# Kernel optimization log

Hardware: AMD Instinct MI355X
Metric: run time of the kernel (lower is better)

## Reference

```python
import jax, jax.numpy as jnp
import numpy as np

W_VV = 0.5  # Eq. 5: mean of video-video and video-text similarity
W_VT = 0.5
MAX_K = 20
EPS = 1e-12  # matches torch.nn.functional.normalize default


def _l2norm(x):
    # normalize along last dim, clamping the norm like F.normalize
    n = jnp.linalg.norm(x, axis=-1, keepdims=True)
    return x / jnp.maximum(n, EPS)


def setup_inputs() -> dict:
    key = jax.random.key(0)
    k1, k2, k3 = jax.random.split(key, 3)
    B, N, D = 64, 100000, 1024
    z_ego = jax.random.normal(k1, (B, D), dtype=jnp.float32)
    exo_bank = jax.random.normal(k2, (N, D), dtype=jnp.float32)
    sim_vt = jax.random.uniform(k3, (N,), dtype=jnp.float32)
    return {"z_ego": z_ego, "exo_bank": exo_bank, "k": 20, "sim_vt": sim_vt}


def reference(z_ego, exo_bank, k, sim_vt):
    N = exo_bank.shape[0]
    k_eff = min(int(k), MAX_K, N)
    # pairwise cosine similarity: [B, N]
    sim_vv = _l2norm(z_ego) @ _l2norm(exo_bank).T
    # broadcast [N] video-text similarity to [B, N]
    sim_vt_b = jnp.broadcast_to(sim_vt[None, :], sim_vv.shape)
    score = W_VV * sim_vv + W_VT * sim_vt_b
    _, topk_idx = jax.lax.top_k(score, k_eff)  # [B, k_eff]
    z_exo = exo_bank[topk_idx]  # [B, k_eff, D]
    return z_exo, topk_idx
```

## Files before the change

kernel.cpp:

```cpp
#include <hip/hip_runtime.h>
#include <math.h>
#include <limits.h>

#define B 64
#define D 1024
#define MAXK 20
#define NSEG 8
#define NT 128
#define KC 64

#define IDX_SENT 0x7FFFFFFF
#define NEG_INF (-INFINITY)

__device__ __forceinline__ bool better(float av, int ai, float bv, int bi) {
    return (av > bv) || (av == bv && ai < bi);
}

__global__ __launch_bounds__(256) void k_norm_ego(const float* __restrict__ ego,
                                                  float* __restrict__ egoN) {
    const int b = blockIdx.x, t = threadIdx.x;
    float4 v = *(const float4*)(ego + (size_t)b * D + t * 4);
    float s = v.x * v.x + v.y * v.y + v.z * v.z + v.w * v.w;
#pragma unroll
    for (int m = 1; m < 64; m <<= 1) s += __shfl_xor(s, m);
    __shared__ float p[4];
    if ((t & 63) == 0) p[t >> 6] = s;
    __syncthreads();
    float tot = p[0] + p[1] + p[2] + p[3];
    float dnm = fmaxf(sqrtf(tot), 1e-12f);
    float4 o;
    o.x = v.x / dnm; o.y = v.y / dnm; o.z = v.z / dnm; o.w = v.w / dnm;
    *(float4*)(egoN + (size_t)b * D + t * 4) = o;
}

__global__ __launch_bounds__(256) void k_scores(const float* __restrict__ exo,
                                                const float* __restrict__ egoN,
                                                const float* __restrict__ svt,
                                                float* __restrict__ scores, int N) {
    __shared__ __align__(16) float eg[64 * 68];
    __shared__ __align__(16) float ex[128 * 64];
    __shared__ float nrm[128];

    const int t = threadIdx.x;
    const int jb = blockIdx.x * NT;
    const int tx = t & 15;
    const int ty = t >> 4;
    const int rr = t >> 4, cc = t & 15;

    float acc[4][8];
#pragma unroll
    for (int m = 0; m < 4; ++m)
#pragma unroll
        for (int i = 0; i < 8; ++i) acc[m][i] = 0.0f;
    float ssq[8] = {0, 0, 0, 0, 0, 0, 0, 0};

    for (int kc = 0; kc < D; kc += KC) {
        __syncthreads();
#pragma unroll
        for (int r = 0; r < 4; ++r) {
            int m = rr + 16 * r;
            float4 v = *(const float4*)(egoN + (size_t)m * D + kc + cc * 4);
            *(float4*)(eg + m * 68 + cc * 4) = v;
        }
#pragma unroll
        for (int r = 0; r < 8; ++r) {
            int j = rr + 16 * r;
            int jj = jb + j;
            float4 v = make_float4(0.f, 0.f, 0.f, 0.f);
            if (jj < N) v = *(const float4*)(exo + (size_t)jj * D + kc + cc * 4);
            ssq[r] += v.x * v.x + v.y * v.y + v.z * v.z + v.w * v.w;
            int cs = cc ^ ((j >> 3) & 7);
            *(float4*)(ex + (j << 6) + (cs << 2)) = v;
        }
        __syncthreads();

        const float* egp = eg + ty * 4 * 68;
#pragma unroll 4
        for (int k4 = 0; k4 < 16; ++k4) {
            float4 a0 = *(const float4*)(egp + 0 * 68 + k4 * 4);
            float4 a1 = *(const float4*)(egp + 1 * 68 + k4 * 4);
            float4 a2 = *(const float4*)(egp + 2 * 68 + k4 * 4);
            float4 a3 = *(const float4*)(egp + 3 * 68 + k4 * 4);
            int ko = (k4 ^ (tx & 7)) << 2;
#pragma unroll
            for (int i = 0; i < 8; ++i) {
                float4 e = *(const float4*)(ex + ((tx * 8 + i) << 6) + ko);
                acc[0][i] += a0.x * e.x; acc[0][i] += a0.y * e.y;
                acc[0][i] += a0.z * e.z; acc[0][i] += a0.w * e.w;
                acc[1][i] += a1.x * e.x; acc[1][i] += a1.y * e.y;
                acc[1][i] += a1.z * e.z; acc[1][i] += a1.w * e.w;
                acc[2][i] += a2.x * e.x; acc[2][i] += a2.y * e.y;
                acc[2][i] += a2.z * e.z; acc[2][i] += a2.w * e.w;
                acc[3][i] += a3.x * e.x; acc[3][i] += a3.y * e.y;
                acc[3][i] += a3.z * e.z; acc[3][i] += a3.w * e.w;
            }
        }
    }

#pragma unroll
    for (int r = 0; r < 8; ++r) {
        float s = ssq[r];
        s += __shfl_xor(s, 1); s += __shfl_xor(s, 2);
        s += __shfl_xor(s, 4); s += __shfl_xor(s, 8);
        if (cc == 0) nrm[rr + 16 * r] = s;
    }
    __syncthreads();

#pragma unroll
    for (int i = 0; i < 8; ++i) {
        int j = tx * 8 + i;
        int jj = jb + j;
        if (jj < N) {
            float dn = fmaxf(sqrtf(nrm[j]), 1e-12f);
            float sv = 0.5f * svt[jj];
#pragma unroll
            for (int m = 0; m < 4; ++m) {
                float sc = 0.5f * (acc[m][i] / dn) + sv;
                scores[(size_t)(ty * 4 + m) * N + jj] = sc;
            }
        }
    }
}

__global__ __launch_bounds__(256) void k_topk_scan(const float* __restrict__ scores,
                                                   float2* __restrict__ cand, int N) {
    const int row = blockIdx.x >> 3;
    const int seg = blockIdx.x & 7;
    const int t = threadIdx.x;
    const int seglen = (N + NSEG - 1) / NSEG;
    const int start = seg * seglen;
    const int end = (start + seglen < N) ? (start + seglen) : N;
    const float* rs = scores + (size_t)row * N;

    float lv[20]; int li[20];
#pragma unroll
    for (int p = 0; p < 20; ++p) { lv[p] = NEG_INF; li[p] = IDX_SENT; }

    for (int j = start + t; j < end; j += 256) {
        float s = rs[j];
        if (s > lv[19] || (s == lv[19] && j < li[19])) {
            float cv = s; int ci = j;
#pragma unroll
            for (int p = 0; p < 20; ++p) {
                bool bb = (cv > lv[p]) || (cv == lv[p] && ci < li[p]);
                float tv = lv[p]; int ti = li[p];
                lv[p] = bb ? cv : tv; li[p] = bb ? ci : ti;
                cv = bb ? tv : cv;   ci = bb ? ti : ci;
            }
        }
    }

    __shared__ float2 wc[4 * 20];
    const int lane = t & 63, w = t >> 6;
#pragma unroll 1
    for (int r = 0; r < 20; ++r) {
        float bv = lv[0]; int bi = li[0];
#pragma unroll
        for (int m = 1; m < 64; m <<= 1) {
            float ov = __shfl_xor(bv, m); int oi = __shfl_xor(bi, m);
            if (better(ov, oi, bv, bi)) { bv = ov; bi = oi; }
        }
        if (lv[0] == bv && li[0] == bi) {
#pragma unroll
            for (int p = 0; p < 19; ++p) { lv[p] = lv[p + 1]; li[p] = li[p + 1]; }
            lv[19] = NEG_INF; li[19] = IDX_SENT;
        }
        if (lane == 0) wc[w * 20 + r] = make_float2(bv, __int_as_float(bi));
    }
    __syncthreads();

    if (w == 0) {
        float mv[2]; int mi[2];
        float2 c0 = (lane < 80) ? wc[lane]
                                : make_float2(NEG_INF, __int_as_float(IDX_SENT));
        float2 c1 = (lane + 64 < 80) ? wc[lane + 64]
                                     : make_float2(NEG_INF, __int_as_float(IDX_SENT));
        mv[0] = c0.x; mi[0] = __float_as_int(c0.y);
        mv[1] = c1.x; mi[1] = __float_as_int(c1.y);
        if (better(mv[1], mi[1], mv[0], mi[0])) {
            float tv = mv[0]; int ti = mi[0];
            mv[0] = mv[1]; mi[0] = mi[1]; mv[1] = tv; mi[1] = ti;
        }
#pragma unroll 1
        for (int r = 0; r < 20; ++r) {
            float bv = mv[0]; int bi = mi[0];
#pragma unroll
            for (int m = 1; m < 64; m <<= 1) {
                float ov = __shfl_xor(bv, m); int oi = __shfl_xor(bi, m);
                if (better(ov, oi, bv, bi)) { bv = ov; bi = oi; }
            }
            if (mv[0] == bv && mi[0] == bi) {
                mv[0] = mv[1]; mi[0] = mi[1];
                mv[1] = NEG_INF; mi[1] = IDX_SENT;
            }
            if (lane == 0)
                cand[((size_t)row * NSEG + seg) * 20 + r] = make_float2(bv, __int_as_float(bi));
        }
    }
}

__global__ __launch_bounds__(64) void k_topk_final(const float2* __restrict__ cand,
                                                   int* __restrict__ idxi,
                                                   float* __restrict__ outIdx) {
    const int row = blockIdx.x;
    const int lane = threadIdx.x;
    const float2* c = cand + (size_t)row * NSEG * 20;

    float mv[3]; int mi[3];
#pragma unroll
    for (int s = 0; s < 3; ++s) { mv[s] = NEG_INF; mi[s] = IDX_SENT; }
#pragma unroll
    for (int s = 0; s < 3; ++s) {
        int ci = lane + 64 * s;
        if (ci < 160) { float2 cc = c[ci]; mv[s] = cc.x; mi[s] = __float_as_int(cc.y); }
    }
    {
        float tv; int ti;
        if (better(mv[1], mi[1], mv[0], mi[0])) { tv = mv[0]; ti = mi[0]; mv[0] = mv[1]; mi[0] = mi[1]; mv[1] = tv; mi[1] = ti; }
        if (better(mv[2], mi[2], mv[1], mi[1])) { tv = mv[1]; ti = mi[1]; mv[1] = mv[2]; mi[1] = mi[2]; mv[2] = tv; mi[2] = ti; }
        if (better(mv[1], mi[1], mv[0], mi[0])) { tv = mv[0]; ti = mi[0]; mv[0] = mv[1]; mi[0] = mi[1]; mv[1] = tv; mi[1] = ti; }
    }
#pragma unroll 1
    for (int r = 0; r < 20; ++r) {
        float bv = mv[0]; int bi = mi[0];
#pragma unroll
        for (int m = 1; m < 64; m <<= 1) {
            float ov = __shfl_xor(bv, m); int oi = __shfl_xor(bi, m);
            if (better(ov, oi, bv, bi)) { bv = ov; bi = oi; }
        }
        if (mv[0] == bv && mi[0] == bi) {
            mv[0] = mv[1]; mi[0] = mi[1];
            mv[1] = mv[2]; mi[1] = mi[2];
            mv[2] = NEG_INF; mi[2] = IDX_SENT;
        }
        if (lane == 0) {
            idxi[row * 20 + r] = bi;
            outIdx[row * 20 + r] = (float)bi;
        }
    }
}

__global__ __launch_bounds__(256) void k_gather(const float* __restrict__ exo,
                                                const int* __restrict__ idxi,
                                                float* __restrict__ out) {
    const int b = blockIdx.x / MAXK, s = blockIdx.x % MAXK;
    const int idx = idxi[b * MAXK + s];
    const float4* src = (const float4*)(exo + (size_t)idx * D);
    float4* dst = (float4*)(out + (size_t)(b * MAXK + s) * D);
    dst[threadIdx.x] = src[threadIdx.x];
}

extern "C" void kernel_launch(void* const* d_in, const int* in_sizes, int n_in,
                              void* d_out, int out_size, void* d_ws, size_t ws_size,
                              hipStream_t stream) {
    (void)n_in; (void)out_size; (void)ws_size;
    const float* ego = (const float*)d_in[0];
    const float* exo = (const float*)d_in[1];
    const float* svt = (const float*)d_in[3];
    const int N = in_sizes[1] / D;

    float* ws = (float*)d_ws;
    float* egoN = ws;
    float* scores = ws + (size_t)B * D;
    float2* cand = (float2*)(scores + (size_t)B * N);
    int* idxi = (int*)(cand + B * NSEG * 20);

    float* out = (float*)d_out;
    float* outIdx = out + (size_t)B * MAXK * D;

    k_norm_ego<<<B, 256, 0, stream>>>(ego, egoN);
    const int nblk = (N + NT - 1) / NT;
    k_scores<<<nblk, 256, 0, stream>>>(exo, egoN, svt, scores, N);
    k_topk_scan<<<B * NSEG, 256, 0, stream>>>(scores, cand, N);
    k_topk_final<<<B, 64, 0, stream>>>(cand, idxi, outIdx);
    k_gather<<<B * MAXK, 256, 0, stream>>>(exo, idxi, out);
}
```

Baseline: 860.6 us.

## Restructure score GEMM tiling with register prefetch and vectorize top-k scan

The score kernel now stages K-major transposed tiles of both operands in shared memory with KC=32. Each thread computes an 8x4 outer-product block from one float4 of exo and two float4s of ego, and the next chunk's global loads are prefetched into registers while the current chunk is computed. The epilogue writes scores as float4, and launch bounds request 4 blocks per CU. The top-k scan reads scores as float4 with 4-aligned segment boundaries, which cuts load instructions but gives each thread four consecutive elements instead of a strided one.

New measurement: 766.6 us. -10.9%, faster.

```diff
diff --git a/kernel.cpp b/kernel.cpp
--- a/kernel.cpp
+++ b/kernel.cpp
@@ -1,13 +1,14 @@
 #include <hip/hip_runtime.h>
 #include <math.h>
-#include <limits.h>
 
 #define B 64
 #define D 1024
 #define MAXK 20
 #define NSEG 8
 #define NT 128
-#define KC 64
+#define KC 32
+#define EXSTRIDE 132
+#define EGSTRIDE 68
 
 #define IDX_SENT 0x7FFFFFFF
 #define NEG_INF (-INFINITY)
@@ -33,91 +34,133 @@
     *(float4*)(egoN + (size_t)b * D + t * 4) = o;
 }
 
-__global__ __launch_bounds__(256) void k_scores(const float* __restrict__ exo,
-                                                const float* __restrict__ egoN,
-                                                const float* __restrict__ svt,
-                                                float* __restrict__ scores, int N) {
-    __shared__ __align__(16) float eg[64 * 68];
-    __shared__ __align__(16) float ex[128 * 64];
-    __shared__ float nrm[128];
+__global__ __launch_bounds__(256, 4) void k_scores(const float* __restrict__ exo,
+                                                   const float* __restrict__ egoN,
+                                                   const float* __restrict__ svt,
+                                                   float* __restrict__ scores, int N) {
+    __shared__ __align__(16) float ex[KC * EXSTRIDE];
+    __shared__ __align__(16) float eg[KC * EGSTRIDE];
+    __shared__ float nrm[NT];
 
     const int t = threadIdx.x;
     const int jb = blockIdx.x * NT;
-    const int tx = t & 15;
-    const int ty = t >> 4;
-    const int rr = t >> 4, cc = t & 15;
-
-    float acc[4][8];
-#pragma unroll
-    for (int m = 0; m < 4; ++m)
-#pragma unroll
-        for (int i = 0; i < 8; ++i) acc[m][i] = 0.0f;
-    float ssq[8] = {0, 0, 0, 0, 0, 0, 0, 0};
-
-    for (int kc = 0; kc < D; kc += KC) {
+    const int tx = t & 31;
+    const int ty = t >> 5;
+    const int jr = t >> 3;
+    const int kq = t & 7;
+
+    float4 acc[8];
+#pragma unroll
+    for (int m = 0; m < 8; ++m) acc[m] = make_float4(0.f, 0.f, 0.f, 0.f);
+    float ssq[4] = {0.f, 0.f, 0.f, 0.f};
+
+    float4 pe[4], pg[2];
+
+    const float4* ex4 = (const float4*)ex;
+    const float4* eg4 = (const float4*)eg;
+
+    {
+        const int kc = 0;
+#pragma unroll
+        for (int q = 0; q < 4; ++q) {
+            int j = jb + jr + 32 * q;
+            pe[q] = (j < N) ? *(const float4*)(exo + (size_t)j * D + kc + kq * 4)
+                            : make_float4(0.f, 0.f, 0.f, 0.f);
+        }
+#pragma unroll
+        for (int p2 = 0; p2 < 2; ++p2) {
+            int m = jr + 32 * p2;
+            pg[p2] = *(const float4*)(egoN + (size_t)m * D + kc + kq * 4);
+        }
+    }
+
+    for (int c = 0; c < D / KC; ++c) {
         __syncthreads();
 #pragma unroll
-        for (int r = 0; r < 4; ++r) {
-            int m = rr + 16 * r;
-            float4 v = *(const float4*)(egoN + (size_t)m * D + kc + cc * 4);
-            *(float4*)(eg + m * 68 + cc * 4) = v;
-        }
-#pragma unroll
-        for (int r = 0; r < 8; ++r) {
-            int j = rr + 16 * r;
-            int jj = jb + j;
-            float4 v = make_float4(0.f, 0.f, 0.f, 0.f);
-            if (jj < N) v = *(const float4*)(exo + (size_t)jj * D + kc + cc * 4);
-            ssq[r] += v.x * v.x + v.y * v.y + v.z * v.z + v.w * v.w;
-            int cs = cc ^ ((j >> 3) & 7);
-            *(float4*)(ex + (j << 6) + (cs << 2)) = v;
+        for (int q = 0; q < 4; ++q) {
+            ssq[q] += pe[q].x * pe[q].x + pe[q].y * pe[q].y +
+                      pe[q].z * pe[q].z + pe[q].w * pe[q].w;
+            int jl = jr + 32 * q;
+            ex[(kq * 4 + 0) * EXSTRIDE + jl] = pe[q].x;
+            ex[(kq * 4 + 1) * EXSTRIDE + jl] = pe[q].y;
+            ex[(kq * 4 + 2) * EXSTRIDE + jl] = pe[q].z;
+            ex[(kq * 4 + 3) * EXSTRIDE + jl] = pe[q].w;
+        }
+#pragma unroll
+        for (int p2 = 0; p2 < 2; ++p2) {
+            int ml = jr + 32 * p2;
+            eg[(kq * 4 + 0) * EGSTRIDE + ml] = pg[p2].x;
+            eg[(kq * 4 + 1) * EGSTRIDE + ml] = pg[p2].y;
+            eg[(kq * 4 + 2) * EGSTRIDE + ml] = pg[p2].z;
+            eg[(kq * 4 + 3) * EGSTRIDE + ml] = pg[p2].w;
         }
         __syncthreads();
-
-        const float* egp = eg + ty * 4 * 68;
-#pragma unroll 4
-        for (int k4 = 0; k4 < 16; ++k4) {
-            float4 a0 = *(const float4*)(egp + 0 * 68 + k4 * 4);
-            float4 a1 = *(const float4*)(egp + 1 * 68 + k4 * 4);
-            float4 a2 = *(const float4*)(egp + 2 * 68 + k4 * 4);
-            float4 a3 = *(const float4*)(egp + 3 * 68 + k4 * 4);
-            int ko = (k4 ^ (tx & 7)) << 2;
-#pragma unroll
-            for (int i = 0; i < 8; ++i) {
-                float4 e = *(const float4*)(ex + ((tx * 8 + i) << 6) + ko);
-                acc[0][i] += a0.x * e.x; acc[0][i] += a0.y * e.y;
-                acc[0][i] += a0.z * e.z; acc[0][i] += a0.w * e.w;
-                acc[1][i] += a1.x * e.x; acc[1][i] += a1.y * e.y;
-                acc[1][i] += a1.z * e.z; acc[1][i] += a1.w * e.w;
-                acc[2][i] += a2.x * e.x; acc[2][i] += a2.y * e.y;
-                acc[2][i] += a2.z * e.z; acc[2][i] += a2.w * e.w;
-                acc[3][i] += a3.x * e.x; acc[3][i] += a3.y * e.y;
-                acc[3][i] += a3.z * e.z; acc[3][i] += a3.w * e.w;
+        if (c + 1 < D / KC) {
+            const int kc = (c + 1) * KC;
+#pragma unroll
+            for (int q = 0; q < 4; ++q) {
+                int j = jb + jr + 32 * q;
+                pe[q] = (j < N) ? *(const float4*)(exo + (size_t)j * D + kc + kq * 4)
+                                : make_float4(0.f, 0.f, 0.f, 0.f);
             }
-        }
-    }
-
-#pragma unroll
-    for (int r = 0; r < 8; ++r) {
-        float s = ssq[r];
-        s += __shfl_xor(s, 1); s += __shfl_xor(s, 2);
-        s += __shfl_xor(s, 4); s += __shfl_xor(s, 8);
-        if (cc == 0) nrm[rr + 16 * r] = s;
+#pragma unroll
+            for (int p2 = 0; p2 < 2; ++p2) {
+                int m = jr + 32 * p2;
+                pg[p2] = *(const float4*)(egoN + (size_t)m * D + kc + kq * 4);
+            }
+        }
+#pragma unroll 8
+        for (int k = 0; k < KC; ++k) {
+            float4 e  = ex4[k * (EXSTRIDE / 4) + tx];
+            float4 a0 = eg4[k * (EGSTRIDE / 4) + (ty << 1)];
+            float4 a1 = eg4[k * (EGSTRIDE / 4) + (ty << 1) + 1];
+            acc[0].x += a0.x * e.x; acc[0].y += a0.x * e.y; acc[0].z += a0.x * e.z; acc[0].w += a0.x * e.w;
+            acc[1].x += a0.y * e.x; acc[1].y += a0.y * e.y; acc[1].z += a0.y * e.z; acc[1].w += a0.y * e.w;
+            acc[2].x += a0.z * e.x; acc[2].y += a0.z * e.y; acc[2].z += a0.z * e.z; acc[2].w += a0.z * e.w;
+            acc[3].x += a0.w * e.x; acc[3].y += a0.w * e.y; acc[3].z += a0.w * e.z; acc[3].w += a0.w * e.w;
+            acc[4].x += a1.x * e.x; acc[4].y += a1.x * e.y; acc[4].z += a1.x * e.z; acc[4].w += a1.x * e.w;
+            acc[5].x += a1.y * e.x; acc[5].y += a1.y * e.y; acc[5].z += a1.y * e.z; acc[5].w += a1.y * e.w;
+            acc[6].x += a1.z * e.x; acc[6].y += a1.z * e.y; acc[6].z += a1.z * e.z; acc[6].w += a1.z * e.w;
+            acc[7].x += a1.w * e.x; acc[7].y += a1.w * e.y; acc[7].z += a1.w * e.z; acc[7].w += a1.w * e.w;
+        }
+    }
+
+#pragma unroll
+    for (int q = 0; q < 4; ++q) {
+        float s = ssq[q];
+        s += __shfl_xor(s, 1); s += __shfl_xor(s, 2); s += __shfl_xor(s, 4);
+        if (kq == 0) nrm[jr + 32 * q] = s;
     }
     __syncthreads();
 
-#pragma unroll
-    for (int i = 0; i < 8; ++i) {
-        int j = tx * 8 + i;
-        int jj = jb + j;
-        if (jj < N) {
-            float dn = fmaxf(sqrtf(nrm[j]), 1e-12f);
-            float sv = 0.5f * svt[jj];
-#pragma unroll
-            for (int m = 0; m < 4; ++m) {
-                float sc = 0.5f * (acc[m][i] / dn) + sv;
-                scores[(size_t)(ty * 4 + m) * N + jj] = sc;
-            }
+    const int j0 = jb + tx * 4;
+    float4 nr = ((const float4*)nrm)[tx];
+    if (j0 + 3 < N) {
+        float4 sv4 = *(const float4*)(svt + j0);
+        float dnx = fmaxf(sqrtf(nr.x), 1e-12f);
+        float dny = fmaxf(sqrtf(nr.y), 1e-12f);
+        float dnz = fmaxf(sqrtf(nr.z), 1e-12f);
+        float dnw = fmaxf(sqrtf(nr.w), 1e-12f);
+#pragma unroll
+        for (int mm = 0; mm < 8; ++mm) {
+            int row = ty * 8 + mm;
+            float4 sc;
+            sc.x = 0.5f * (acc[mm].x / dnx) + 0.5f * sv4.x;
+            sc.y = 0.5f * (acc[mm].y / dny) + 0.5f * sv4.y;
+            sc.z = 0.5f * (acc[mm].z / dnz) + 0.5f * sv4.z;
+            sc.w = 0.5f * (acc[mm].w / dnw) + 0.5f * sv4.w;
+            *(float4*)(scores + (size_t)row * N + j0) = sc;
+        }
+    } else if (j0 < N) {
+        float dn[4] = {fmaxf(sqrtf(nr.x), 1e-12f), fmaxf(sqrtf(nr.y), 1e-12f),
+                       fmaxf(sqrtf(nr.z), 1e-12f), fmaxf(sqrtf(nr.w), 1e-12f)};
+#pragma unroll
+        for (int mm = 0; mm < 8; ++mm) {
+            int row = ty * 8 + mm;
+            if (j0 + 0 < N) scores[(size_t)row * N + j0 + 0] = 0.5f * (acc[mm].x / dn[0]) + 0.5f * svt[j0 + 0];
+            if (j0 + 1 < N) scores[(size_t)row * N + j0 + 1] = 0.5f * (acc[mm].y / dn[1]) + 0.5f * svt[j0 + 1];
+            if (j0 + 2 < N) scores[(size_t)row * N + j0 + 2] = 0.5f * (acc[mm].z / dn[2]) + 0.5f * svt[j0 + 2];
+            if (j0 + 3 < N) scores[(size_t)row * N + j0 + 3] = 0.5f * (acc[mm].w / dn[3]) + 0.5f * svt[j0 + 3];
         }
     }
 }
@@ -127,7 +170,8 @@
     const int row = blockIdx.x >> 3;
     const int seg = blockIdx.x & 7;
     const int t = threadIdx.x;
-    const int seglen = (N + NSEG - 1) / NSEG;
+    int seglen = (N + NSEG - 1) / NSEG;
+    seglen = (seglen + 3) & ~3;
     const int start = seg * seglen;
     const int end = (start + seglen < N) ? (start + seglen) : N;
     const float* rs = scores + (size_t)row * N;
@@ -136,19 +180,36 @@
 #pragma unroll
     for (int p = 0; p < 20; ++p) { lv[p] = NEG_INF; li[p] = IDX_SENT; }
 
-    for (int j = start + t; j < end; j += 256) {
-        float s = rs[j];
-        if (s > lv[19] || (s == lv[19] && j < li[19])) {
-            float cv = s; int ci = j;
-#pragma unroll
-            for (int p = 0; p < 20; ++p) {
-                bool bb = (cv > lv[p]) || (cv == lv[p] && ci < li[p]);
-                float tv = lv[p]; int ti = li[p];
-                lv[p] = bb ? cv : tv; li[p] = bb ? ci : ti;
-                cv = bb ? tv : cv;   ci = bb ? ti : ci;
-            }
-        }
-    }
+#define TK_INSERT(SVAL, JIDX)                                                     \
+    if ((SVAL) > lv[19] || ((SVAL) == lv[19] && (JIDX) < li[19])) {               \
+        float cv = (SVAL); int ci = (JIDX);                                       \
+        _Pragma("unroll")                                                         \
+        for (int p = 0; p < 20; ++p) {                                            \
+            bool bb = (cv > lv[p]) || (cv == lv[p] && ci < li[p]);                \
+            float tv = lv[p]; int ti = li[p];                                     \
+            lv[p] = bb ? cv : tv; li[p] = bb ? ci : ti;                           \
+            cv = bb ? tv : cv;   ci = bb ? ti : ci;                               \
+        }                                                                         \
+    }
+
+    if (start < end) {
+        const int end4 = end & ~3;
+        const float4* rs4 = (const float4*)rs;
+        for (int jf = (start >> 2) + t; jf < (end4 >> 2); jf += 256) {
+            float4 f = rs4[jf];
+            int j0 = jf << 2;
+            TK_INSERT(f.x, j0);
+            TK_INSERT(f.y, j0 + 1);
+            TK_INSERT(f.z, j0 + 2);
+            TK_INSERT(f.w, j0 + 3);
+        }
+        if (t < end - end4) {
+            int j = end4 + t;
+            float s = rs[j];
+            TK_INSERT(s, j);
+        }
+    }
+#undef TK_INSERT
 
     __shared__ float2 wc[4 * 20];
     const int lane = t & 63, w = t >> 6;
```
